# Kernel tuning notes

Hardware: AMD Instinct MI355X
Metric: run time of the kernel (lower is better)

Reference implementation:

```python
import jax, jax.numpy as jnp
import numpy as np
from jax import lax

N, C_IN, DIMS, NW, T, H, W = 8, 64, 64, 8, 16, 64, 64
BN_EPS = 1e-5


def setup_inputs() -> dict:
    key = jax.random.key(0)
    ks = jax.random.split(key, 10)
    # kaiming-ish scales
    w_scale = (2.0 / (C_IN * 27)) ** 0.5
    return {
        "x": jax.random.normal(ks[0], (N, C_IN, T, H, W), dtype=jnp.float32),
        "weights": jax.random.normal(ks[1], (NW, DIMS, C_IN, 3, 3, 3), dtype=jnp.float32) * w_scale,
        "biases": jax.random.normal(ks[2], (NW, DIMS), dtype=jnp.float32),
        "se_w1": jax.random.normal(ks[3], (16, C_IN, 5, 5), dtype=jnp.float32) * (2.0 / (C_IN * 25)) ** 0.5,
        "se_b1": jnp.zeros((16,), dtype=jnp.float32),
        "se_w2": jax.random.normal(ks[4], (32, 16, 5, 5), dtype=jnp.float32) * (2.0 / (16 * 25)) ** 0.5,
        "se_b2": jnp.zeros((32,), dtype=jnp.float32),
        "lin_w": jax.random.normal(ks[5], (NW, 32), dtype=jnp.float32) * (1.0 / 32) ** 0.5,
        "lin_b": jnp.zeros((NW,), dtype=jnp.float32),
        "bn_gamma": jnp.ones((DIMS,), dtype=jnp.float32),
        "bn_beta": jnp.zeros((DIMS,), dtype=jnp.float32),
        "epochs_num": 15,
    }


def _forward(x, weights, biases, se_w1, se_b1, se_w2, se_b2, lin_w, lin_b, bn_gamma, bn_beta, epochs_num):
    tau = 30.0 - 2.9 * epochs_num if epochs_num < 10 else 1.0
    # std over temporal axis (torch.std -> unbiased, ddof=1): [n, c, h, w]
    std_x = jnp.std(x, axis=2, ddof=1)
    # squeeze-expand attention branch
    dn2d = ("NCHW", "OIHW", "NCHW")
    h1 = lax.conv_general_dilated(std_x, se_w1, (1, 1), "VALID", dimension_numbers=dn2d)
    h1 = jax.nn.relu(h1 + se_b1[None, :, None, None])
    h2 = lax.conv_general_dilated(h1, se_w2, (1, 1), "VALID", dimension_numbers=dn2d)
    h2 = jax.nn.relu(h2 + se_b2[None, :, None, None])
    pooled = jnp.max(h2, axis=(2, 3))                      # [n, 32]
    logits = pooled @ lin_w.T + lin_b                       # [n, num_weights]
    phi = jax.nn.softmax(logits / tau, axis=1)
    # per-sample dynamic kernels / biases
    dyn_w = jnp.einsum("bn,ncidhw->bcidhw", phi, weights)   # [n, dims, c_in, 3,3,3]
    dyn_b = phi @ biases                                    # [n, dims]
    # grouped conv3d (groups = n) == per-sample conv3d via vmap
    dn3d = ("NCDHW", "OIDHW", "NCDHW")
    def one_conv(xi, wi):
        return lax.conv_general_dilated(xi[None], wi, (1, 1, 1), "SAME", dimension_numbers=dn3d)[0]
    y = jax.vmap(one_conv)(x, dyn_w)                        # [n, dims, t, h, w]
    y = y + dyn_b[:, :, None, None, None]
    # BatchNorm3d (training mode, batch stats, biased var)
    mean = jnp.mean(y, axis=(0, 2, 3, 4))
    var = jnp.var(y, axis=(0, 2, 3, 4))
    b = lambda v: v[None, :, None, None, None]
    y = (y - b(mean)) * b(bn_gamma) * lax.rsqrt(b(var) + BN_EPS) + b(bn_beta)
    return jax.nn.relu(y)


def reference(x, weights, biases, se_w1, se_b1, se_w2, se_b2, lin_w, lin_b, bn_gamma, bn_beta, epochs_num):
    return _forward(x, weights, biases, se_w1, se_b1, se_w2, se_b2, lin_w, lin_b, bn_gamma, bn_beta, epochs_num)
```

## Files before the change

### kernel.cpp

```cpp
#include <hip/hip_runtime.h>
#include <hip/hip_bf16.h>
#include <math.h>

#define N_   8
#define CIN_ 64
#define DIMS_ 64
#define NW_  8
#define T_   16
#define H_   64
#define W_   64
#define HW_  (H_ * W_)
#define THW_ (T_ * HW_)

typedef short bf16x8 __attribute__((ext_vector_type(8)));
typedef float f32x16 __attribute__((ext_vector_type(16)));

__device__ __forceinline__ unsigned short f2bf(float f) {
    union { float f; unsigned u; } a; a.f = f;
    unsigned r = a.u + 0x7fffu + ((a.u >> 16) & 1u);
    return (unsigned short)(r >> 16);
}

#define CS8_ 8
#define HS8_ (66 * CS8_)
#define TS8_ (10 * HS8_)
#define XSH_ (3 * TS8_)
#define WLH_ (28 * 64 * 8)

__host__ __device__ constexpr int OXc(int tap) {
    int tt = tap > 26 ? 26 : tap;
    return (tt / 9) * TS8_ + ((tt % 9) / 3) * HS8_ + ((tt % 3) - 1) * CS8_;
}

__global__ __launch_bounds__(512) void stdxb_kernel(
    const float* __restrict__ x, float* __restrict__ std_x,
    unsigned short* __restrict__ xb)
{
    __shared__ unsigned short xsl[16 * 64 * 8];
    const int h = blockIdx.x, c8 = blockIdx.y, n = blockIdx.z;
    const int tid = threadIdx.x;
    const int c = tid >> 6, w = tid & 63;
    const int cin = c8 * 8 + c;
    const float* px = x + (((size_t)(n * 64 + cin)) << 16) + (h << 6) + w;
    float s = 0.f, s2 = 0.f;
#pragma unroll
    for (int t = 0; t < T_; ++t) {
        float v = px[t * HW_];
        s += v;
        s2 += v * v;
        xsl[(t << 9) + (w << 3) + c] = f2bf(v);
    }
    float var = (s2 - s * s * (1.0f / 16.0f)) * (1.0f / 15.0f);
    std_x[(((size_t)(n * 64 + cin)) << 12) + (h << 6) + w] = sqrtf(fmaxf(var, 0.f));
    __syncthreads();
    const int4* src = (const int4*)xsl;
    int4* dst = (int4*)(xb + ((size_t)((n * 8 + c8) * 16) << 12) * 8);
#pragma unroll
    for (int k = 0; k < 2; ++k) {
        int j = tid + (k << 9);
        int t = j >> 6, ww = j & 63;
        dst[((t << 6) + h) * 64 + ww] = src[j];
    }
}

__global__ void wtrans(const float* __restrict__ w1, const float* __restrict__ w2,
                       float* __restrict__ w1t, float* __restrict__ w2t) {
    int i = blockIdx.x * 256 + threadIdx.x;
    if (i < 25600) {
        int k = i / 1600, c = (i / 25) % 64, tap = i % 25;
        w1t[(c * 25 + tap) * 16 + k] = w1[i];
    } else if (i < 38400) {
        int j = i - 25600;
        int o = j / 400, c = (j / 25) % 16, tap = j % 25;
        w2t[(c * 25 + tap) * 32 + o] = w2[j];
    }
}

__global__ __launch_bounds__(256) void se_conv1c(const float* __restrict__ std_x,
        const float* __restrict__ w1t, const float* __restrict__ b1, float* __restrict__ h1) {
    __shared__ float red[3][64][8];
    const int n = blockIdx.y, ks = blockIdx.z * 8;
    const int iq = threadIdx.x & 63, cq = threadIdx.x >> 6;
    const int ij = blockIdx.x * 64 + iq;
    float acc[8];
#pragma unroll
    for (int q = 0; q < 8; ++q) acc[q] = 0.f;
    if (ij < 3600) {
        int i = ij / 60, j = ij - i * 60;
        const float* xn = std_x + (size_t)n * CIN_ * HW_ + i * W_ + j;
        for (int c = cq * 16; c < cq * 16 + 16; ++c) {
            const float* xc = xn + c * HW_;
            float xv[25];
#pragma unroll
            for (int u = 0; u < 5; ++u)
#pragma unroll
                for (int v = 0; v < 5; ++v) xv[u * 5 + v] = xc[u * W_ + v];
            const float* wc = w1t + c * 400 + ks;
#pragma unroll
            for (int tap = 0; tap < 25; ++tap)
#pragma unroll
                for (int q = 0; q < 8; ++q)
                    acc[q] = fmaf(xv[tap], wc[tap * 16 + q], acc[q]);
        }
    }
    if (cq > 0) {
#pragma unroll
        for (int q = 0; q < 8; ++q) red[cq - 1][iq][q] = acc[q];
    }
    __syncthreads();
    if (cq == 0 && ij < 3600) {
#pragma unroll
        for (int q = 0; q < 8; ++q) {
            float a = acc[q] + red[0][iq][q] + red[1][iq][q] + red[2][iq][q] + b1[ks + q];
            h1[((size_t)(n * 16 + ks + q)) * 3600 + ij] = fmaxf(a, 0.f);
        }
    }
}

__global__ __launch_bounds__(256) void se_conv2c(const float* __restrict__ h1,
        const float* __restrict__ w2t, const float* __restrict__ b2,
        unsigned* __restrict__ pooled) {
    __shared__ float red[3][64][8];
    const int n = blockIdx.y, os = blockIdx.z * 8;
    const int iq = threadIdx.x & 63, cq = threadIdx.x >> 6;
    const int ij = blockIdx.x * 64 + iq;
    const int i = ij / 56, j = ij - i * 56;
    float acc[8];
#pragma unroll
    for (int q = 0; q < 8; ++q) acc[q] = 0.f;
    const float* xn = h1 + (size_t)n * 16 * 3600 + i * 60 + j;
    for (int c = cq * 4; c < cq * 4 + 4; ++c) {
        const float* xc = xn + c * 3600;
        float xv[25];
#pragma unroll
        for (int u = 0; u < 5; ++u)
#pragma unroll
            for (int v = 0; v < 5; ++v) xv[u * 5 + v] = xc[u * 60 + v];
        const float* wc = w2t + c * 800 + os;
#pragma unroll
        for (int tap = 0; tap < 25; ++tap)
#pragma unroll
            for (int q = 0; q < 8; ++q)
                acc[q] = fmaf(xv[tap], wc[tap * 32 + q], acc[q]);
    }
    if (cq > 0) {
#pragma unroll
        for (int q = 0; q < 8; ++q) red[cq - 1][iq][q] = acc[q];
    }
    __syncthreads();
    if (cq == 0) {
#pragma unroll
        for (int q = 0; q < 8; ++q) {
            float a = fmaxf(acc[q] + red[0][iq][q] + red[1][iq][q] + red[2][iq][q] + b2[os + q], 0.f);
#pragma unroll
            for (int m = 1; m < 64; m <<= 1) a = fmaxf(a, __shfl_xor(a, m, 64));
            if (iq == 0) atomicMax(&pooled[n * 32 + os + q], __float_as_uint(a));
        }
    }
}

__global__ void se_head(const float* __restrict__ pooled, const float* __restrict__ lin_w,
                        const float* __restrict__ lin_b, const float* __restrict__ biases,
                        const int* __restrict__ epochs, float* __restrict__ phi,
                        float* __restrict__ dyn_b) {
    __shared__ float sphi[NW_][NW_];
    int tid = threadIdx.x;
    int e = epochs[0];
    float tau = (e < 10) ? (30.0f - 2.9f * (float)e) : 1.0f;
    if (tid < 64) {
        int b = tid >> 3, m = tid & 7;
        float acc = lin_b[m];
        for (int k = 0; k < 32; ++k) acc += pooled[b * 32 + k] * lin_w[m * 32 + k];
        sphi[b][m] = acc / tau;
    }
    __syncthreads();
    if (tid < 8) {
        int b = tid;
        float mx = sphi[b][0];
#pragma unroll
        for (int m = 1; m < 8; ++m) mx = fmaxf(mx, sphi[b][m]);
        float ex[8], s = 0.f;
#pragma unroll
        for (int m = 0; m < 8; ++m) { ex[m] = expf(sphi[b][m] - mx); s += ex[m]; }
        float inv = 1.0f / s;
#pragma unroll
        for (int m = 0; m < 8; ++m) { sphi[b][m] = ex[m] * inv; phi[b * 8 + m] = ex[m] * inv; }
    }
    __syncthreads();
    for (int idx = tid; idx < NW_ * DIMS_; idx += blockDim.x) {
        int b = idx >> 6, d = idx & 63;
        float acc = 0.f;
#pragma unroll
        for (int m = 0; m < 8; ++m) acc += sphi[b][m] * biases[m * DIMS_ + d];
        dyn_b[idx] = acc;
    }
}

__global__ void dyn_w_bf16b(const float* __restrict__ weights, const float* __restrict__ phi,
                            unsigned short* __restrict__ wtb2) {
    int g = blockIdx.x * 256 + threadIdx.x;
    int b = blockIdx.y;
    int c8 = g / 14336, r = g - c8 * 14336;
    int tap = r >> 9, co = (r >> 3) & 63, ci = r & 7;
    int cin = c8 * 8 + ci;
    unsigned short v = 0;
    if (tap < 27) {
        size_t src = ((size_t)(co * 64) + cin) * 27 + tap;
        float acc = 0.f;
#pragma unroll
        for (int m = 0; m < 8; ++m)
            acc += phi[b * 8 + m] * weights[(size_t)m * (64 * 64 * 27) + src];
        v = f2bf(acc);
    }
    wtb2[(size_t)b * 114688 + g] = v;
}

__global__ __launch_bounds__(512, 4) void conv3d_mfma3(
    const unsigned short* __restrict__ xb,
    const unsigned short* __restrict__ wtb2,
    const float* __restrict__ dynb,
    float* __restrict__ y,
    float* __restrict__ sums)
{
    __shared__ __align__(16) unsigned short xs[XSH_];
    __shared__ __align__(16) unsigned short wl[WLH_];
    __shared__ float bnred[128];

    const int hb = blockIdx.x, t = blockIdx.y, n = blockIdx.z;
    const int tid = threadIdx.x;
    const int lane = tid & 63, wid = tid >> 6;
    const int lane31 = lane & 31, tau = lane >> 5;
    const int hbase = hb * 8;

    for (int i = tid; i < XSH_ / 8; i += 512)
        *(int4*)&xs[i * 8] = (int4){0, 0, 0, 0};
    if (tid < 128) bnred[tid] = 0.f;

    const unsigned short* xnb = xb + ((size_t)(n * 8) << 16) * 8;
    const unsigned short* wnb = wtb2 + (size_t)n * 114688;

    f32x16 acc[2][2];
#pragma unroll
    for (int ci = 0; ci < 2; ++ci)
#pragma unroll
        for (int s = 0; s < 2; ++s)
            acc[ci][s] = (f32x16)(0.f);

    const int aBase = (tau * 64 + lane31) * 8;
    const int bsp0 = wid * HS8_ + (1 + lane31) * CS8_;
    const int bsp1 = bsp0 + 32 * CS8_;

    for (int c8 = 0; c8 < 8; ++c8) {
        __syncthreads();
#pragma unroll
        for (int k = 0; k < 4; ++k) {
            int r = wid + (k << 3);
            if (r < 30) {
                int tp = (r >= 20) ? 2 : (r >= 10 ? 1 : 0);
                int hp = r - tp * 10;
                int gt = t + tp - 1, gh = hbase + hp - 1;
                if (((unsigned)gt < 16u) && ((unsigned)gh < 64u)) {
                    const unsigned short* gp = xnb + (size_t)(((c8 * 16 + gt) * 64 + gh) * 64 + lane) * 8;
                    const unsigned short* lp = &xs[tp * TS8_ + hp * HS8_ + CS8_];
                    __builtin_amdgcn_global_load_lds(
                        (const __attribute__((address_space(1))) void*)gp,
                        (__attribute__((address_space(3))) void*)lp, 16, 0, 0);
                }
            }
        }
#pragma unroll
        for (int k = 0; k < 4; ++k) {
            int tp = wid + (k << 3);
            if (tp < 28) {
                const unsigned short* gp = wnb + (size_t)(c8 * 14336 + tp * 512 + lane * 8);
                const unsigned short* lp = &wl[tp * 512];
                __builtin_amdgcn_global_load_lds(
                    (const __attribute__((address_space(1))) void*)gp,
                    (__attribute__((address_space(3))) void*)lp, 16, 0, 0);
            }
        }
        __syncthreads();

#pragma unroll
        for (int p = 0; p < 14; ++p) {
            const int xo = tau ? OXc(2 * p + 1) : OXc(2 * p);
            bf16x8 a0 = *(const bf16x8*)&wl[p * 1024 + aBase];
            bf16x8 a1 = *(const bf16x8*)&wl[p * 1024 + aBase + 256];
            bf16x8 b0 = *(const bf16x8*)&xs[bsp0 + xo];
            bf16x8 b1 = *(const bf16x8*)&xs[bsp1 + xo];
            acc[0][0] = __builtin_amdgcn_mfma_f32_32x32x16_bf16(a0, b0, acc[0][0], 0, 0, 0);
            acc[0][1] = __builtin_amdgcn_mfma_f32_32x32x16_bf16(a0, b1, acc[0][1], 0, 0, 0);
            acc[1][0] = __builtin_amdgcn_mfma_f32_32x32x16_bf16(a1, b0, acc[1][0], 0, 0, 0);
            acc[1][1] = __builtin_amdgcn_mfma_f32_32x32x16_bf16(a1, b1, acc[1][1], 0, 0, 0);
        }
    }

    const float* db = dynb + n * DIMS_;
    const size_t ybase = (((size_t)n * DIMS_) << 16) + ((size_t)t << 12) + ((size_t)(hbase + wid) << 6);
#pragma unroll
    for (int ci = 0; ci < 2; ++ci) {
#pragma unroll
        for (int r = 0; r < 16; ++r) {
            const int co = 32 * ci + (r & 3) + 8 * (r >> 2) + 4 * tau;
            const float bco = db[co];
            float z0 = acc[ci][0][r] + bco;
            float z1 = acc[ci][1][r] + bco;
            y[ybase + ((size_t)co << 16) + lane31]      = z0;
            y[ybase + ((size_t)co << 16) + 32 + lane31] = z1;
            float ps = z0 + z1, ps2 = z0 * z0 + z1 * z1;
#pragma unroll
            for (int m = 1; m < 32; m <<= 1) {
                ps += __shfl_xor(ps, m, 64);
                ps2 += __shfl_xor(ps2, m, 64);
            }
            if (lane31 == 0) {
                atomicAdd(&bnred[co], ps);
                atomicAdd(&bnred[64 + co], ps2);
            }
        }
    }
    __syncthreads();
    if (tid < 128) atomicAdd(&sums[tid], bnred[tid]);
}

__global__ void bn_norm4(const float* __restrict__ sums, const float* __restrict__ gamma,
                         const float* __restrict__ beta, float* __restrict__ y) {
    size_t idx = (size_t)blockIdx.x * 256 + threadIdx.x;
    int c = (int)((idx >> 14) & 63);
    const float cnt = (float)(N_ * THW_);
    float mean = sums[c] / cnt;
    float var = sums[64 + c] / cnt - mean * mean;
    float sc = gamma[c] * rsqrtf(var + 1e-5f);
    float sh = beta[c] - mean * sc;
    float4 v = ((float4*)y)[idx];
    v.x = fmaxf(fmaf(v.x, sc, sh), 0.f);
    v.y = fmaxf(fmaf(v.y, sc, sh), 0.f);
    v.z = fmaxf(fmaf(v.z, sc, sh), 0.f);
    v.w = fmaxf(fmaf(v.w, sc, sh), 0.f);
    ((float4*)y)[idx] = v;
}

extern "C" void kernel_launch(void* const* d_in, const int* in_sizes, int n_in,
                              void* d_out, int out_size, void* d_ws, size_t ws_size,
                              hipStream_t stream) {
    const float* x       = (const float*)d_in[0];
    const float* weights = (const float*)d_in[1];
    const float* biases  = (const float*)d_in[2];
    const float* se_w1   = (const float*)d_in[3];
    const float* se_b1   = (const float*)d_in[4];
    const float* se_w2   = (const float*)d_in[5];
    const float* se_b2   = (const float*)d_in[6];
    const float* lin_w   = (const float*)d_in[7];
    const float* lin_b   = (const float*)d_in[8];
    const float* gamma   = (const float*)d_in[9];
    const float* beta    = (const float*)d_in[10];
    const int*   epochs  = (const int*)d_in[11];

    float* out = (float*)d_out;
    float* ws = (float*)d_ws;

    const size_t STD_OFF  = 0;
    const size_t H1_OFF   = STD_OFF + 2097152;
    const size_t SUMS_OFF = H1_OFF + 460800;
    const size_t POOL_OFF = SUMS_OFF + 128;
    const size_t PHI_OFF  = POOL_OFF + 256;
    const size_t DYNB_OFF = PHI_OFF + 64;
    const size_t WTB_OFF  = DYNB_OFF + 512;
    const size_t W1T_OFF  = WTB_OFF + 458752;
    const size_t W2T_OFF  = W1T_OFF + 25600;
    const size_t XB_OFF   = W2T_OFF + 12800;

    float* std_x  = ws + STD_OFF;
    float* h1     = ws + H1_OFF;
    float* sums   = ws + SUMS_OFF;
    float* pooled = ws + POOL_OFF;
    float* phi    = ws + PHI_OFF;
    float* dynb   = ws + DYNB_OFF;
    unsigned short* wtb2 = (unsigned short*)(ws + WTB_OFF);
    float* w1t    = ws + W1T_OFF;
    float* w2t    = ws + W2T_OFF;
    unsigned short* xb = (unsigned short*)(ws + XB_OFF);

    hipMemsetAsync(sums, 0, (128 + 256) * sizeof(float), stream);

    stdxb_kernel<<<dim3(64, 8, 8), 512, 0, stream>>>(x, std_x, xb);
    wtrans<<<150, 256, 0, stream>>>(se_w1, se_w2, w1t, w2t);

    se_conv1c<<<dim3(57, 8, 2), 256, 0, stream>>>(std_x, w1t, se_b1, h1);
    se_conv2c<<<dim3(49, 8, 4), 256, 0, stream>>>(h1, w2t, se_b2, (unsigned*)pooled);
    se_head<<<1, 64, 0, stream>>>(pooled, lin_w, lin_b, biases, epochs, phi, dynb);

    dyn_w_bf16b<<<dim3(448, 8), 256, 0, stream>>>(weights, phi, wtb2);

    conv3d_mfma3<<<dim3(8, 16, 8), 512, 0, stream>>>(xb, wtb2, dynb, out, sums);

    bn_norm4<<<32768, 256, 0, stream>>>(sums, gamma, beta, out);
}
```

Measured before the change: 408.5 us.

## Fuse SE head into dynamic-weight kernel, widen conv tiles per wave, grid-stride BN

Several changes are bundled. The memset is folded into the first kernel, and the softmax head is merged with the dynamic-weight mixing so each thread reads eight source weights once and writes all eight samples' outputs. The conv3d kernel moves to 256 threads, with each wave computing four spatial tiles instead of two, which raises MFMA reuse of the A fragments but doubles accumulator registers. BN normalization becomes a grid-stride loop over fewer blocks. Risks include register pressure in the conv and scattered bf16 writes in the weight kernel.

Result: faster. 372.2 us (-8.9%).

```diff
diff --git a/kernel.cpp b/kernel.cpp
--- a/kernel.cpp
+++ b/kernel.cpp
@@ -34,11 +34,16 @@
 
 __global__ __launch_bounds__(512) void stdxb_kernel(
     const float* __restrict__ x, float* __restrict__ std_x,
-    unsigned short* __restrict__ xb)
+    unsigned short* __restrict__ xb, float* __restrict__ sums,
+    unsigned* __restrict__ pooled)
 {
     __shared__ unsigned short xsl[16 * 64 * 8];
     const int h = blockIdx.x, c8 = blockIdx.y, n = blockIdx.z;
     const int tid = threadIdx.x;
+    if ((blockIdx.x | blockIdx.y | blockIdx.z) == 0) {
+        if (tid < 128) sums[tid] = 0.f;
+        else if (tid < 384) pooled[tid - 128] = 0u;
+    }
     const int c = tid >> 6, w = tid & 63;
     const int cin = c8 * 8 + c;
     const float* px = x + (((size_t)(n * 64 + cin)) << 16) + (h << 6) + w;
@@ -159,63 +164,68 @@
     }
 }
 
-__global__ void se_head(const float* __restrict__ pooled, const float* __restrict__ lin_w,
-                        const float* __restrict__ lin_b, const float* __restrict__ biases,
-                        const int* __restrict__ epochs, float* __restrict__ phi,
-                        float* __restrict__ dyn_b) {
-    __shared__ float sphi[NW_][NW_];
-    int tid = threadIdx.x;
-    int e = epochs[0];
-    float tau = (e < 10) ? (30.0f - 2.9f * (float)e) : 1.0f;
+__global__ __launch_bounds__(256) void dyn_w_head(
+    const float* __restrict__ weights, const float* __restrict__ pooled,
+    const float* __restrict__ lin_w, const float* __restrict__ lin_b,
+    const float* __restrict__ biases, const int* __restrict__ epochs,
+    unsigned short* __restrict__ wtb2, float* __restrict__ dyn_b) {
+    __shared__ float slog[8][8];
+    __shared__ float sphi[64];
+    const int tid = threadIdx.x;
+    const int e = epochs[0];
+    const float tau = (e < 10) ? (30.0f - 2.9f * (float)e) : 1.0f;
     if (tid < 64) {
         int b = tid >> 3, m = tid & 7;
         float acc = lin_b[m];
+#pragma unroll
         for (int k = 0; k < 32; ++k) acc += pooled[b * 32 + k] * lin_w[m * 32 + k];
-        sphi[b][m] = acc / tau;
+        slog[b][m] = acc / tau;
     }
     __syncthreads();
     if (tid < 8) {
-        int b = tid;
-        float mx = sphi[b][0];
-#pragma unroll
-        for (int m = 1; m < 8; ++m) mx = fmaxf(mx, sphi[b][m]);
-        float ex[8], s = 0.f;
-#pragma unroll
-        for (int m = 0; m < 8; ++m) { ex[m] = expf(sphi[b][m] - mx); s += ex[m]; }
-        float inv = 1.0f / s;
-#pragma unroll
-        for (int m = 0; m < 8; ++m) { sphi[b][m] = ex[m] * inv; phi[b * 8 + m] = ex[m] * inv; }
-    }
-    __syncthreads();
-    for (int idx = tid; idx < NW_ * DIMS_; idx += blockDim.x) {
-        int b = idx >> 6, d = idx & 63;
+        float mx = slog[tid][0];
+#pragma unroll
+        for (int m = 1; m < 8; ++m) mx = fmaxf(mx, slog[tid][m]);
+        float ex[8], ssum = 0.f;
+#pragma unroll
+        for (int m = 0; m < 8; ++m) { ex[m] = expf(slog[tid][m] - mx); ssum += ex[m]; }
+        float inv = 1.0f / ssum;
+#pragma unroll
+        for (int m = 0; m < 8; ++m) sphi[tid * 8 + m] = ex[m] * inv;
+    }
+    __syncthreads();
+    if (blockIdx.x < 64) {
+        int b = blockIdx.x >> 3, c8 = blockIdx.x & 7;
+        unsigned* dst = (unsigned*)(wtb2 + (size_t)b * 114688 + (size_t)(c8 * 28 + 27) * 512);
+        dst[tid] = 0u;
+    }
+    if (blockIdx.x == 0) {
+#pragma unroll
+        for (int idx = tid; idx < 512; idx += 256) {
+            int b = idx >> 6, d = idx & 63;
+            float a = 0.f;
+#pragma unroll
+            for (int m = 0; m < 8; ++m) a += sphi[b * 8 + m] * biases[m * DIMS_ + d];
+            dyn_b[idx] = a;
+        }
+    }
+    int f = blockIdx.x * 256 + tid;
+    if (f >= 110592) return;
+    int tap = f % 27, cin = (f / 27) & 63, co = f / 1728;
+    float wv[8];
+#pragma unroll
+    for (int m = 0; m < 8; ++m) wv[m] = weights[(size_t)m * 110592 + f];
+    size_t dbase = (size_t)(cin >> 3) * 14336 + tap * 512 + co * 8 + (cin & 7);
+#pragma unroll
+    for (int b = 0; b < 8; ++b) {
         float acc = 0.f;
 #pragma unroll
-        for (int m = 0; m < 8; ++m) acc += sphi[b][m] * biases[m * DIMS_ + d];
-        dyn_b[idx] = acc;
-    }
-}
-
-__global__ void dyn_w_bf16b(const float* __restrict__ weights, const float* __restrict__ phi,
-                            unsigned short* __restrict__ wtb2) {
-    int g = blockIdx.x * 256 + threadIdx.x;
-    int b = blockIdx.y;
-    int c8 = g / 14336, r = g - c8 * 14336;
-    int tap = r >> 9, co = (r >> 3) & 63, ci = r & 7;
-    int cin = c8 * 8 + ci;
-    unsigned short v = 0;
-    if (tap < 27) {
-        size_t src = ((size_t)(co * 64) + cin) * 27 + tap;
-        float acc = 0.f;
-#pragma unroll
-        for (int m = 0; m < 8; ++m)
-            acc += phi[b * 8 + m] * weights[(size_t)m * (64 * 64 * 27) + src];
-        v = f2bf(acc);
-    }
-    wtb2[(size_t)b * 114688 + g] = v;
-}
-
-__global__ __launch_bounds__(512, 4) void conv3d_mfma3(
+        for (int m = 0; m < 8; ++m) acc += sphi[b * 8 + m] * wv[m];
+        wtb2[(size_t)b * 114688 + dbase] = f2bf(acc);
+    }
+}
+
+__global__ __launch_bounds__(256, 2) void conv3d_mfma5(
     const unsigned short* __restrict__ xb,
     const unsigned short* __restrict__ wtb2,
     const float* __restrict__ dynb,
@@ -232,29 +242,40 @@
     const int lane31 = lane & 31, tau = lane >> 5;
     const int hbase = hb * 8;
 
-    for (int i = tid; i < XSH_ / 8; i += 512)
+    for (int i = tid; i < XSH_ / 8; i += 256)
         *(int4*)&xs[i * 8] = (int4){0, 0, 0, 0};
     if (tid < 128) bnred[tid] = 0.f;
 
-    const unsigned short* xnb = xb + ((size_t)(n * 8) << 16) * 8;
+    const unsigned short* xnb = xb + (size_t)n * 4194304;
     const unsigned short* wnb = wtb2 + (size_t)n * 114688;
 
-    f32x16 acc[2][2];
+    f32x16 acc[2][4];
 #pragma unroll
     for (int ci = 0; ci < 2; ++ci)
 #pragma unroll
-        for (int s = 0; s < 2; ++s)
+        for (int s = 0; s < 4; ++s)
             acc[ci][s] = (f32x16)(0.f);
 
-    const int aBase = (tau * 64 + lane31) * 8;
-    const int bsp0 = wid * HS8_ + (1 + lane31) * CS8_;
-    const int bsp1 = bsp0 + 32 * CS8_;
+    const int aBase = tau * 512 + lane31 * 8;
+    int bsp[4];
+#pragma unroll
+    for (int s = 0; s < 4; ++s)
+        bsp[s] = (2 * wid + (s >> 1)) * HS8_ + (1 + (s & 1) * 32 + lane31) * CS8_;
 
     for (int c8 = 0; c8 < 8; ++c8) {
         __syncthreads();
 #pragma unroll
-        for (int k = 0; k < 4; ++k) {
-            int r = wid + (k << 3);
+        for (int k = 0; k < 7; ++k) {
+            int tp = wid + (k << 2);
+            const unsigned short* gp = wnb + ((size_t)c8 * 14336 + tp * 512 + lane * 8);
+            const unsigned short* lp = &wl[tp * 512];
+            __builtin_amdgcn_global_load_lds(
+                (const __attribute__((address_space(1))) void*)gp,
+                (__attribute__((address_space(3))) void*)lp, 16, 0, 0);
+        }
+#pragma unroll
+        for (int k = 0; k < 8; ++k) {
+            int r = wid + (k << 2);
             if (r < 30) {
                 int tp = (r >= 20) ? 2 : (r >= 10 ? 1 : 0);
                 int hp = r - tp * 10;
@@ -268,17 +289,6 @@
                 }
             }
         }
-#pragma unroll
-        for (int k = 0; k < 4; ++k) {
-            int tp = wid + (k << 3);
-            if (tp < 28) {
-                const unsigned short* gp = wnb + (size_t)(c8 * 14336 + tp * 512 + lane * 8);
-                const unsigned short* lp = &wl[tp * 512];
-                __builtin_amdgcn_global_load_lds(
-                    (const __attribute__((address_space(1))) void*)gp,
-                    (__attribute__((address_space(3))) void*)lp, 16, 0, 0);
-            }
-        }
         __syncthreads();
 
 #pragma unroll
@@ -286,28 +296,38 @@
             const int xo = tau ? OXc(2 * p + 1) : OXc(2 * p);
             bf16x8 a0 = *(const bf16x8*)&wl[p * 1024 + aBase];
             bf16x8 a1 = *(const bf16x8*)&wl[p * 1024 + aBase + 256];
-            bf16x8 b0 = *(const bf16x8*)&xs[bsp0 + xo];
-            bf16x8 b1 = *(const bf16x8*)&xs[bsp1 + xo];
+            bf16x8 b0 = *(const bf16x8*)&xs[bsp[0] + xo];
+            bf16x8 b1 = *(const bf16x8*)&xs[bsp[1] + xo];
+            bf16x8 b2 = *(const bf16x8*)&xs[bsp[2] + xo];
+            bf16x8 b3 = *(const bf16x8*)&xs[bsp[3] + xo];
             acc[0][0] = __builtin_amdgcn_mfma_f32_32x32x16_bf16(a0, b0, acc[0][0], 0, 0, 0);
             acc[0][1] = __builtin_amdgcn_mfma_f32_32x32x16_bf16(a0, b1, acc[0][1], 0, 0, 0);
+            acc[0][2] = __builtin_amdgcn_mfma_f32_32x32x16_bf16(a0, b2, acc[0][2], 0, 0, 0);
+            acc[0][3] = __builtin_amdgcn_mfma_f32_32x32x16_bf16(a0, b3, acc[0][3], 0, 0, 0);
             acc[1][0] = __builtin_amdgcn_mfma_f32_32x32x16_bf16(a1, b0, acc[1][0], 0, 0, 0);
             acc[1][1] = __builtin_amdgcn_mfma_f32_32x32x16_bf16(a1, b1, acc[1][1], 0, 0, 0);
+            acc[1][2] = __builtin_amdgcn_mfma_f32_32x32x16_bf16(a1, b2, acc[1][2], 0, 0, 0);
+            acc[1][3] = __builtin_amdgcn_mfma_f32_32x32x16_bf16(a1, b3, acc[1][3], 0, 0, 0);
         }
     }
 
     const float* db = dynb + n * DIMS_;
-    const size_t ybase = (((size_t)n * DIMS_) << 16) + ((size_t)t << 12) + ((size_t)(hbase + wid) << 6);
 #pragma unroll
     for (int ci = 0; ci < 2; ++ci) {
 #pragma unroll
         for (int r = 0; r < 16; ++r) {
             const int co = 32 * ci + (r & 3) + 8 * (r >> 2) + 4 * tau;
             const float bco = db[co];
-            float z0 = acc[ci][0][r] + bco;
-            float z1 = acc[ci][1][r] + bco;
-            y[ybase + ((size_t)co << 16) + lane31]      = z0;
-            y[ybase + ((size_t)co << 16) + 32 + lane31] = z1;
-            float ps = z0 + z1, ps2 = z0 * z0 + z1 * z1;
+            float ps = 0.f, ps2 = 0.f;
+#pragma unroll
+            for (int s = 0; s < 4; ++s) {
+                float z = acc[ci][s][r] + bco;
+                size_t yi = ((size_t)(n * 64 + co) << 16) + ((size_t)t << 12)
+                          + ((size_t)(hbase + 2 * wid + (s >> 1)) << 6) + (s & 1) * 32 + lane31;
+                y[yi] = z;
+                ps += z;
+                ps2 += z * z;
+            }
 #pragma unroll
             for (int m = 1; m < 32; m <<= 1) {
                 ps += __shfl_xor(ps, m, 64);
@@ -325,19 +345,21 @@
 
 __global__ void bn_norm4(const float* __restrict__ sums, const float* __restrict__ gamma,
                          const float* __restrict__ beta, float* __restrict__ y) {
-    size_t idx = (size_t)blockIdx.x * 256 + threadIdx.x;
-    int c = (int)((idx >> 14) & 63);
     const float cnt = (float)(N_ * THW_);
-    float mean = sums[c] / cnt;
-    float var = sums[64 + c] / cnt - mean * mean;
-    float sc = gamma[c] * rsqrtf(var + 1e-5f);
-    float sh = beta[c] - mean * sc;
-    float4 v = ((float4*)y)[idx];
-    v.x = fmaxf(fmaf(v.x, sc, sh), 0.f);
-    v.y = fmaxf(fmaf(v.y, sc, sh), 0.f);
-    v.z = fmaxf(fmaf(v.z, sc, sh), 0.f);
-    v.w = fmaxf(fmaf(v.w, sc, sh), 0.f);
-    ((float4*)y)[idx] = v;
+    for (size_t idx = (size_t)blockIdx.x * 256 + threadIdx.x; idx < 8388608;
+         idx += (size_t)4096 * 256) {
+        int c = (int)((idx >> 14) & 63);
+        float mean = sums[c] / cnt;
+        float var = sums[64 + c] / cnt - mean * mean;
+        float sc = gamma[c] * rsqrtf(var + 1e-5f);
+        float sh = beta[c] - mean * sc;
+        float4 v = ((float4*)y)[idx];
+        v.x = fmaxf(fmaf(v.x, sc, sh), 0.f);
+        v.y = fmaxf(fmaf(v.y, sc, sh), 0.f);
+        v.z = fmaxf(fmaf(v.z, sc, sh), 0.f);
+        v.w = fmaxf(fmaf(v.w, sc, sh), 0.f);
+        ((float4*)y)[idx] = v;
+    }
 }
 
 extern "C" void kernel_launch(void* const* d_in, const int* in_sizes, int n_in,
@@ -374,25 +396,22 @@
     float* h1     = ws + H1_OFF;
     float* sums   = ws + SUMS_OFF;
     float* pooled = ws + POOL_OFF;
-    float* phi    = ws + PHI_OFF;
     float* dynb   = ws + DYNB_OFF;
     unsigned short* wtb2 = (unsigned short*)(ws + WTB_OFF);
     float* w1t    = ws + W1T_OFF;
     float* w2t    = ws + W2T_OFF;
     unsigned short* xb = (unsigned short*)(ws + XB_OFF);
 
-    hipMemsetAsync(sums, 0, (128 + 256) * sizeof(float), stream);
-
-    stdxb_kernel<<<dim3(64, 8, 8), 512, 0, stream>>>(x, std_x, xb);
+    stdxb_kernel<<<dim3(64, 8, 8), 512, 0, stream>>>(x, std_x, xb, sums, (unsigned*)pooled);
     wtrans<<<150, 256, 0, stream>>>(se_w1, se_w2, w1t, w2t);
 
     se_conv1c<<<dim3(57, 8, 2), 256, 0, stream>>>(std_x, w1t, se_b1, h1);
     se_conv2c<<<dim3(49, 8, 4), 256, 0, stream>>>(h1, w2t, se_b2, (unsigned*)pooled);
-    se_head<<<1, 64, 0, stream>>>(pooled, lin_w, lin_b, biases, epochs, phi, dynb);
-
-    dyn_w_bf16b<<<dim3(448, 8), 256, 0, stream>>>(weights, phi, wtb2);
-
-    conv3d_mfma3<<<dim3(8, 16, 8), 512, 0, stream>>>(xb, wtb2, dynb, out, sums);
-
-    bn_norm4<<<32768, 256, 0, stream>>>(sums, gamma, beta, out);
-}
+
+    dyn_w_head<<<432, 256, 0, stream>>>(weights, pooled, lin_w, lin_b, biases, epochs,
+                                        wtb2, dynb);
+
+    conv3d_mfma5<<<dim3(8, 16, 8), 256, 0, stream>>>(xb, wtb2, dynb, out, sums);
+
+    bn_norm4<<<4096, 256, 0, stream>>>(sums, gamma, beta, out);
+}
```
